# Kernel tuning notes

Measured on AMD Instinct MI355X. Metric: run time of the kernel, lower is better.

## Reference

```python
import jax, jax.numpy as jnp
import numpy as np

NEG_BIG = -9.0e15  # mask value from original code (-9000000000000000.0)


def setup_inputs() -> dict:
    key = jax.random.key(0)
    k1, k2, k3, k4, k5 = jax.random.split(key, 5)
    B, N, M, D = 32, 1024, 1024, 128
    input1 = jax.random.normal(k1, (B, N, D), dtype=jnp.float32)
    input2 = jax.random.normal(k2, (B, M, D), dtype=jnp.float32)
    adj = jax.random.randint(k3, (B, N, M), 0, 2, dtype=jnp.int32)
    # xavier_normal on (D,1): std = gain*sqrt(2/(fan_in+fan_out)) = 1.414*sqrt(2/(D+1))
    std = 1.414 * np.sqrt(2.0 / (D + 1))
    a1 = jax.random.normal(k4, (D, 1), dtype=jnp.float32) * std
    a2 = jax.random.normal(k5, (D, 1), dtype=jnp.float32) * std
    return {"input1": input1, "input2": input2, "adj": adj, "a1": a1, "a2": a2}


def reference(input1, input2, adj, a1, a2):
    h, g = input1, input2
    # e1: (B,N,1), e2: (B,1,M); broadcast add replaces the repeat() calls
    e1 = jnp.matmul(h, a1)                      # (B,N,1)
    e2 = jnp.matmul(g, a2).transpose(0, 2, 1)   # (B,1,M)
    e = jax.nn.leaky_relu(e1 + e2, negative_slope=0.2)  # (B,N,M)
    attention = jnp.where(adj > 0, e, NEG_BIG)
    attention = jax.nn.softmax(attention, axis=2)
    attention = jnp.where(jnp.isnan(attention), 0.0, attention)
    # per-batch loop in original builds adj_[b,i,j] = adj[b,i,:].sum(); vectorized:
    deg = jnp.sum(adj, axis=2, keepdims=True).astype(attention.dtype)  # (B,N,1)
    attention = attention * deg
    h_prime = jnp.matmul(attention, g)          # (B,N,D)
    return h_prime
```

## Files before the change

kernel.cpp:

```cpp
#include <hip/hip_runtime.h>

#define BB 32
#define NN 1024
#define MM 1024
#define DD 128

typedef __attribute__((ext_vector_type(4))) float f32x4;
typedef __attribute__((ext_vector_type(8))) __bf16 bf16x8;
typedef unsigned short ushort_t;
typedef unsigned int uint_t;

#define L2E 1.44269504f
#define KEXP 9.357623e-14f
#define KEXPINV 1.0686475e13f

__device__ __forceinline__ unsigned f2bf(float x) {
    unsigned u = __builtin_bit_cast(unsigned, x);
    return (u + 0x7fffu + ((u >> 16) & 1u)) >> 16;
}

#define GLOAD16(gp, lp)                                                     \
    __builtin_amdgcn_global_load_lds(                                       \
        (const __attribute__((address_space(1))) unsigned int*)(gp),        \
        (__attribute__((address_space(3))) unsigned int*)(lp), 16, 0, 0)

__global__ __launch_bounds__(256) void prep(
    const float* __restrict__ g, const float* __restrict__ h,
    const float* __restrict__ a1, const float* __restrict__ a2,
    ushort_t* __restrict__ gq, float* __restrict__ e1, float* __restrict__ e2)
{
    __shared__ ushort_t tl[DD][66];
    int b = blockIdx.y, m0 = blockIdx.x * 64, t = threadIdx.x;

    #pragma unroll
    for (int i = 0; i < 8; i++) {
        int idx = i * 256 + t;
        int m = idx >> 5;
        int c4 = (idx & 31) * 4;
        float4 v = *(const float4*)(h + ((size_t)(b * NN + m0 + m)) * DD + c4);
        float4 av = *(const float4*)(a1 + c4);
        float p = v.x * av.x + v.y * av.y + v.z * av.z + v.w * av.w;
        #pragma unroll
        for (int s = 16; s; s >>= 1) p += __shfl_xor(p, s);
        if ((t & 31) == 0) e1[b * NN + m0 + m] = p;
    }
    #pragma unroll
    for (int i = 0; i < 8; i++) {
        int idx = i * 256 + t;
        int m = idx >> 5;
        int c4 = (idx & 31) * 4;
        float4 v = *(const float4*)(g + ((size_t)(b * MM + m0 + m)) * DD + c4);
        tl[c4 + 0][m] = (ushort_t)f2bf(v.x);
        tl[c4 + 1][m] = (ushort_t)f2bf(v.y);
        tl[c4 + 2][m] = (ushort_t)f2bf(v.z);
        tl[c4 + 3][m] = (ushort_t)f2bf(v.w);
        float4 av = *(const float4*)(a2 + c4);
        float p = v.x * av.x + v.y * av.y + v.z * av.z + v.w * av.w;
        #pragma unroll
        for (int s = 16; s; s >>= 1) p += __shfl_xor(p, s);
        if ((t & 31) == 0) e2[b * MM + m0 + m] = p;
    }
    __syncthreads();
    #pragma unroll
    for (int i = 0; i < 4; i++) {
        int idx = i * 256 + t;
        int d = idx >> 3;
        int c = (idx & 7) * 8;
        int4 o;
        o.x = (int)((unsigned)tl[d][c + 0] | ((unsigned)tl[d][c + 1] << 16));
        o.y = (int)((unsigned)tl[d][c + 2] | ((unsigned)tl[d][c + 3] << 16));
        o.z = (int)((unsigned)tl[d][c + 4] | ((unsigned)tl[d][c + 5] << 16));
        o.w = (int)((unsigned)tl[d][c + 6] | ((unsigned)tl[d][c + 7] << 16));
        int mg = m0 + c;
        *(int4*)(gq + (((size_t)((b * 32 + (mg >> 5)) * DD + d)) << 5) + (mg & 31)) = o;
    }
}

__global__ __launch_bounds__(256) void attn_tiled(
    const int* __restrict__ adj, const ushort_t* __restrict__ gq,
    const float* __restrict__ e1, const float* __restrict__ e2,
    float* __restrict__ out)
{
    __shared__ __align__(16) float e2S[MM];
    __shared__ __align__(16) int adjS[2][64 * 32];
    __shared__ __align__(16) ushort_t gqS[2][32 * 128];

    int b = blockIdx.y, n0 = blockIdx.x * 64, t = threadIdx.x;
    int wid = t >> 6, lane = t & 63;
    int rlo = lane & 15, hh = lane >> 4;
    int r = wid * 16 + rlo;
    int r8 = r & 7;

    {
        float4 ev = *(const float4*)(e2 + b * MM + t * 4);
        ev.x *= L2E; ev.y *= L2E; ev.z *= L2E; ev.w *= L2E;
        *(float4*)(&e2S[t * 4]) = ev;
    }
    float e1f = L2E * e1[b * NN + n0 + r];

    const int* adjb = adj + (size_t)(b * NN + n0) * MM;
    const ushort_t* gqb = gq + (size_t)b * (32 * DD * 32);

    int di0 = t, di1 = t + 256;
    int row0 = di0 >> 3, slot0 = di0 & 7, seg0 = slot0 ^ (row0 & 7);
    int row1 = di1 >> 3, slot1 = di1 & 7, seg1 = slot1 ^ (row1 & 7);

#define STAGE(P, K) do {                                                    \
        GLOAD16(adjb + (size_t)row0 * MM + (K) * 32 + seg0 * 4,             \
                &adjS[P][di0 * 4]);                                         \
        GLOAD16(adjb + (size_t)row1 * MM + (K) * 32 + seg1 * 4,             \
                &adjS[P][di1 * 4]);                                         \
        GLOAD16(gqb + (size_t)(K) * 4096 + di0 * 8, &gqS[P][di0 * 8]);      \
        GLOAD16(gqb + (size_t)(K) * 4096 + di1 * 8, &gqS[P][di1 * 8]);      \
    } while (0)

    f32x4 acc[8];
    #pragma unroll
    for (int j = 0; j < 8; j++) acc[j] = (f32x4){0.f, 0.f, 0.f, 0.f};
    float zl = 0.f, dl = 0.f;

    STAGE(0, 0);
    asm volatile("s_waitcnt vmcnt(0)");
    __syncthreads();

    for (int k = 0; k < 32; ++k) {
        int p = k & 1;
        if (k < 31) STAGE(p ^ 1, k + 1);

        int4 a0 = *(const int4*)(&adjS[p][r * 32 + ((2 * hh) ^ r8) * 4]);
        int4 a1 = *(const int4*)(&adjS[p][r * 32 + ((2 * hh + 1) ^ r8) * 4]);
        float4 ev0 = *(const float4*)(&e2S[k * 32 + 8 * hh]);
        float4 ev1 = *(const float4*)(&e2S[k * 32 + 8 * hh + 4]);
        float ex[8] = {ev0.x, ev0.y, ev0.z, ev0.w, ev1.x, ev1.y, ev1.z, ev1.w};
        int   ax[8] = {a0.x, a0.y, a0.z, a0.w, a1.x, a1.y, a1.z, a1.w};

        bf16x8 af;
        #pragma unroll
        for (int jj = 0; jj < 8; jj++) {
            float sp = e1f + ex[jj];
            float lk = fmaxf(sp, 0.2f * sp);
            float sel = (ax[jj] > 0) ? KEXP : 0.f;
            float wv = sel * __builtin_amdgcn_exp2f(lk);
            zl += wv;
            dl += sel;
            af[jj] = (__bf16)wv;
        }
        #pragma unroll
        for (int j = 0; j < 8; j++) {
            int4 bv = *(const int4*)(&gqS[p][(j * 16 + rlo) * 32 + 8 * hh]);
            acc[j] = __builtin_amdgcn_mfma_f32_16x16x32_bf16(
                         af, __builtin_bit_cast(bf16x8, bv), acc[j], 0, 0, 0);
        }

        asm volatile("s_waitcnt vmcnt(0)");
        __syncthreads();
    }
#undef STAGE

    zl += __shfl_xor(zl, 16); zl += __shfl_xor(zl, 32);
    dl += __shfl_xor(dl, 16); dl += __shfl_xor(dl, 32);
    float sc = (dl > 0.f) ? (dl * KEXPINV) / zl : 0.f;

    float scr[4];
    #pragma unroll
    for (int rg = 0; rg < 4; rg++) scr[rg] = __shfl(sc, 4 * hh + rg);

    float* ob = out + ((size_t)(b * NN + n0 + wid * 16)) * DD + rlo;
    #pragma unroll
    for (int j = 0; j < 8; j++)
        #pragma unroll
        for (int rg = 0; rg < 4; rg++)
            ob[(size_t)(4 * hh + rg) * DD + j * 16] = acc[j][rg] * scr[rg];
}

extern "C" void kernel_launch(void* const* d_in, const int* in_sizes, int n_in,
                              void* d_out, int out_size, void* d_ws, size_t ws_size,
                              hipStream_t stream) {
    const float* h   = (const float*)d_in[0];
    const float* g   = (const float*)d_in[1];
    const int*   adj = (const int*)d_in[2];
    const float* a1  = (const float*)d_in[3];
    const float* a2  = (const float*)d_in[4];
    float* out = (float*)d_out;

    char* ws = (char*)d_ws;
    float*    e1 = (float*)(ws);
    float*    e2 = (float*)(ws + (128u << 10));
    ushort_t* gq = (ushort_t*)(ws + (512u << 10));

    prep<<<dim3(MM / 64, BB), 256, 0, stream>>>(g, h, a1, a2, gq, e1, e2);
    attn_tiled<<<dim3(NN / 64, BB), 256, 0, stream>>>(adj, gq, e1, e2, out);
}
```

Before: 51.91 us.

## Deepen attention load pipeline to four LDS stages and swizzle gq tiles

Replaces the double-buffered adj/gq staging with a four-buffer ring that keeps three stages of global loads in flight. Each iteration now does a partial vmcnt wait and a single barrier instead of a full drain, so more HBM traffic overlaps the softmax-weight and MFMA compute. It also XOR-swizzles the gq tile layout in LDS to cut bank conflicts on the B-operand reads. The cost is roughly double the LDS per block and a hand-written vmcnt schedule that must stay exactly in step with the four loads per stage.

After: 48.09 us. 7.4% less time.

```diff
diff --git a/kernel.cpp b/kernel.cpp
--- a/kernel.cpp
+++ b/kernel.cpp
@@ -76,14 +76,14 @@
     }
 }
 
-__global__ __launch_bounds__(256) void attn_tiled(
+__global__ __launch_bounds__(256, 2) void attn_tiled(
     const int* __restrict__ adj, const ushort_t* __restrict__ gq,
     const float* __restrict__ e1, const float* __restrict__ e2,
     float* __restrict__ out)
 {
     __shared__ __align__(16) float e2S[MM];
-    __shared__ __align__(16) int adjS[2][64 * 32];
-    __shared__ __align__(16) ushort_t gqS[2][32 * 128];
+    __shared__ __align__(16) int adjS[4][64 * 32];
+    __shared__ __align__(16) ushort_t gqS[4][128 * 32];
 
     int b = blockIdx.y, n0 = blockIdx.x * 64, t = threadIdx.x;
     int wid = t >> 6, lane = t & 63;
@@ -97,21 +97,26 @@
         *(float4*)(&e2S[t * 4]) = ev;
     }
     float e1f = L2E * e1[b * NN + n0 + r];
+    __syncthreads();
 
     const int* adjb = adj + (size_t)(b * NN + n0) * MM;
     const ushort_t* gqb = gq + (size_t)b * (32 * DD * 32);
 
-    int di0 = t, di1 = t + 256;
-    int row0 = di0 >> 3, slot0 = di0 & 7, seg0 = slot0 ^ (row0 & 7);
-    int row1 = di1 >> 3, slot1 = di1 & 7, seg1 = slot1 ^ (row1 & 7);
+    int adi0 = t, adi1 = t + 256;
+    int arow0 = adi0 >> 3, aseg0 = (adi0 & 7) ^ (arow0 & 7);
+    int arow1 = adi1 >> 3, aseg1 = (adi1 & 7) ^ (arow1 & 7);
+    int gd0 = adi0 >> 2, gseg0 = (adi0 & 3) ^ ((gd0 >> 1) & 3);
+    int gd1 = adi1 >> 2, gseg1 = (adi1 & 3) ^ ((gd1 >> 1) & 3);
 
 #define STAGE(P, K) do {                                                    \
-        GLOAD16(adjb + (size_t)row0 * MM + (K) * 32 + seg0 * 4,             \
-                &adjS[P][di0 * 4]);                                         \
-        GLOAD16(adjb + (size_t)row1 * MM + (K) * 32 + seg1 * 4,             \
-                &adjS[P][di1 * 4]);                                         \
-        GLOAD16(gqb + (size_t)(K) * 4096 + di0 * 8, &gqS[P][di0 * 8]);      \
-        GLOAD16(gqb + (size_t)(K) * 4096 + di1 * 8, &gqS[P][di1 * 8]);      \
+        GLOAD16(adjb + (size_t)arow0 * MM + (K) * 32 + aseg0 * 4,           \
+                &adjS[P][adi0 * 4]);                                        \
+        GLOAD16(adjb + (size_t)arow1 * MM + (K) * 32 + aseg1 * 4,           \
+                &adjS[P][adi1 * 4]);                                        \
+        GLOAD16(gqb + (size_t)(K) * 4096 + gd0 * 32 + gseg0 * 8,            \
+                &gqS[P][adi0 * 8]);                                         \
+        GLOAD16(gqb + (size_t)(K) * 4096 + gd1 * 32 + gseg1 * 8,            \
+                &gqS[P][adi1 * 8]);                                         \
     } while (0)
 
     f32x4 acc[8];
@@ -119,42 +124,54 @@
     for (int j = 0; j < 8; j++) acc[j] = (f32x4){0.f, 0.f, 0.f, 0.f};
     float zl = 0.f, dl = 0.f;
 
-    STAGE(0, 0);
-    asm volatile("s_waitcnt vmcnt(0)");
-    __syncthreads();
-
-    for (int k = 0; k < 32; ++k) {
-        int p = k & 1;
-        if (k < 31) STAGE(p ^ 1, k + 1);
-
-        int4 a0 = *(const int4*)(&adjS[p][r * 32 + ((2 * hh) ^ r8) * 4]);
-        int4 a1 = *(const int4*)(&adjS[p][r * 32 + ((2 * hh + 1) ^ r8) * 4]);
-        float4 ev0 = *(const float4*)(&e2S[k * 32 + 8 * hh]);
-        float4 ev1 = *(const float4*)(&e2S[k * 32 + 8 * hh + 4]);
-        float ex[8] = {ev0.x, ev0.y, ev0.z, ev0.w, ev1.x, ev1.y, ev1.z, ev1.w};
-        int   ax[8] = {a0.x, a0.y, a0.z, a0.w, a1.x, a1.y, a1.z, a1.w};
-
-        bf16x8 af;
-        #pragma unroll
-        for (int jj = 0; jj < 8; jj++) {
-            float sp = e1f + ex[jj];
-            float lk = fmaxf(sp, 0.2f * sp);
-            float sel = (ax[jj] > 0) ? KEXP : 0.f;
-            float wv = sel * __builtin_amdgcn_exp2f(lk);
-            zl += wv;
-            dl += sel;
-            af[jj] = (__bf16)wv;
-        }
-        #pragma unroll
-        for (int j = 0; j < 8; j++) {
-            int4 bv = *(const int4*)(&gqS[p][(j * 16 + rlo) * 32 + 8 * hh]);
-            acc[j] = __builtin_amdgcn_mfma_f32_16x16x32_bf16(
-                         af, __builtin_bit_cast(bf16x8, bv), acc[j], 0, 0, 0);
-        }
-
-        asm volatile("s_waitcnt vmcnt(0)");
-        __syncthreads();
-    }
+#define COMPUTE(P, K) do {                                                  \
+        int4 a0 = *(const int4*)(&adjS[P][r * 32 + ((2 * hh) ^ r8) * 4]);   \
+        int4 a1 = *(const int4*)(&adjS[P][r * 32 + ((2 * hh + 1) ^ r8) * 4]);\
+        float4 ev0 = *(const float4*)(&e2S[(K) * 32 + 8 * hh]);             \
+        float4 ev1 = *(const float4*)(&e2S[(K) * 32 + 8 * hh + 4]);         \
+        float ex[8] = {ev0.x, ev0.y, ev0.z, ev0.w,                          \
+                       ev1.x, ev1.y, ev1.z, ev1.w};                         \
+        int   ax[8] = {a0.x, a0.y, a0.z, a0.w, a1.x, a1.y, a1.z, a1.w};     \
+        bf16x8 af;                                                          \
+        _Pragma("unroll")                                                   \
+        for (int jj = 0; jj < 8; jj++) {                                    \
+            float sp = e1f + ex[jj];                                        \
+            float lk = fmaxf(sp, 0.2f * sp);                                \
+            float sel = (ax[jj] > 0) ? KEXP : 0.f;                          \
+            float wv = sel * __builtin_amdgcn_exp2f(lk);                    \
+            zl += wv;                                                       \
+            dl += sel;                                                      \
+            af[jj] = (__bf16)wv;                                            \
+        }                                                                   \
+        _Pragma("unroll")                                                   \
+        for (int j = 0; j < 8; j++) {                                       \
+            int d = j * 16 + rlo;                                           \
+            int4 bv = *(const int4*)(                                       \
+                &gqS[P][d * 32 + (hh ^ ((rlo >> 1) & 3)) * 8]);             \
+            acc[j] = __builtin_amdgcn_mfma_f32_16x16x32_bf16(               \
+                         af, __builtin_bit_cast(bf16x8, bv), acc[j], 0,0,0);\
+        }                                                                   \
+    } while (0)
+
+    STAGE(0, 0); STAGE(1, 1); STAGE(2, 2);
+
+    for (int k = 0; k < 30; ++k) {
+        asm volatile("s_waitcnt vmcnt(8)" ::: "memory");
+        __builtin_amdgcn_s_barrier();
+        __builtin_amdgcn_sched_barrier(0);
+        if (k < 29) STAGE((k + 3) & 3, k + 3);
+        COMPUTE(k & 3, k);
+    }
+    asm volatile("s_waitcnt vmcnt(4)" ::: "memory");
+    __builtin_amdgcn_s_barrier();
+    __builtin_amdgcn_sched_barrier(0);
+    COMPUTE(2, 30);
+    asm volatile("s_waitcnt vmcnt(0)" ::: "memory");
+    __builtin_amdgcn_s_barrier();
+    __builtin_amdgcn_sched_barrier(0);
+    COMPUTE(3, 31);
+
+#undef COMPUTE
 #undef STAGE
 
     zl += __shfl_xor(zl, 16); zl += __shfl_xor(zl, 32);
```
